# Optimization experiments

Hardware: AMD Instinct MI355X
Metric: run time of the kernel (lower is better)

Reference implementation:

```python
import jax, jax.numpy as jnp
import numpy as np

N = 50000      # num nodes
E = 800000     # num edges
F = 64         # in_channels
H = 4          # heads
C = 64         # out_channels
NEG_SLOPE = 0.2
SCALE = float(np.sqrt(F))  # scaled_product=True -> divide by sqrt(in_channels)


def setup_inputs() -> dict:
    key = jax.random.key(0)
    k1, k2, k3, k4, k5, k6 = jax.random.split(key, 6)
    x = jax.random.normal(k1, (N, F), dtype=jnp.float32)
    edge_index = jax.random.randint(k2, (2, E), 0, N, dtype=jnp.int32)
    edge_weight = jax.random.uniform(k3, (E, 1), dtype=jnp.float32)
    # learned parameters (glorot-ish scale)
    W_lin = jax.random.normal(k4, (F, H * C), dtype=jnp.float32) / np.sqrt(F)
    W_att = jax.random.normal(k5, (F, H * F), dtype=jnp.float32) / np.sqrt(F)
    bias = jnp.zeros((H * C,), dtype=jnp.float32)
    return {"x": x, "edge_index": edge_index, "edge_weight": edge_weight,
            "W_lin": W_lin, "W_att": W_att, "bias": bias}


def reference(x, edge_index, edge_weight, W_lin, W_att, bias):
    src = edge_index[0]  # j: source / message sender
    dst = edge_index[1]  # i: target / aggregation index

    # node transforms
    xs = (x @ W_lin).reshape(N, H, C)   # lin(x): values for messages
    u = (x @ W_att).reshape(N, H, F)    # lin_att(x): multiplicative attention keys

    # multiplicative attention score: x_j^T W_h x_i  -> [E, H]
    score = jnp.einsum('ehf,ef->eh', u[src], x[dst]) / SCALE
    score = jax.nn.leaky_relu(score, NEG_SLOPE)

    # masked scatter-softmax over incoming edges of each destination node
    smax = jax.ops.segment_max(jax.lax.stop_gradient(score), dst, num_segments=N)  # [N, H]
    e = jnp.exp(score - smax[dst]) * edge_weight                                   # mask = edge_weight
    denom = jax.ops.segment_sum(e, dst, num_segments=N) + 1e-16                    # [N, H]
    alpha = e / denom[dst]                                                         # [E, H]

    # message = alpha * x_src, aggregate (add) at destination
    out = jax.ops.segment_sum(alpha[:, :, None] * xs[src], dst, num_segments=N)    # [N, H, C]
    out = out.reshape(N, H * C) + bias                                             # concat heads + bias
    return out
```

## Files before the change

### kernel.cpp

```cpp
#include <hip/hip_runtime.h>
#include <hip/hip_bf16.h>
#include <math.h>

#define N_NODES 50000
#define N_EDGES 800000
#define GEMM_ROWS 32
#define AGG_NODES 32
#define PAD_EDGES (N_EDGES + N_NODES * 15)
#define QGEMM_BLOCKS ((N_NODES + GEMM_ROWS - 1) / GEMM_ROWS)
#define BASE_BLOCKS ((N_NODES + 255) / 256)
#define SCALE_FOLD 0.18033688011112042f
#define XT_STRIDE 36

typedef __attribute__((ext_vector_type(8))) short bf16x8_t;
typedef __attribute__((ext_vector_type(4))) float f32x4_t;

static __device__ __forceinline__ ushort bfrn(float v) {
  __hip_bfloat16 b = __float2bfloat16(v);
  return __builtin_bit_cast(ushort, b);
}
static __device__ __forceinline__ bf16x8_t as_bf16x8(uint4 u) {
  union { uint4 a; bf16x8_t b; } c; c.a = u; return c.b;
}
static __device__ __forceinline__ float bflo(uint u) {
  return __uint_as_float(u << 16);
}
static __device__ __forceinline__ float bfhi(uint u) {
  return __uint_as_float(u & 0xFFFF0000u);
}

__global__ __launch_bounds__(256) void hist_kernel(
    const int* __restrict__ dst, int* __restrict__ deg, int* __restrict__ epos,
    const float* __restrict__ Watt, float* __restrict__ Wt) {
  int e = blockIdx.x * 256 + threadIdx.x;
  if (e < 16384) {
    int c = e & 63;
    int r = (e >> 6) & 63;
    int h = e >> 12;
    Wt[e] = Watt[c * 256 + h * 64 + r] * SCALE_FOLD;
  }
  if (e < N_EDGES) epos[e] = atomicAdd(&deg[dst[e]], 1);
}

__global__ __launch_bounds__(256) void qgemm_base_kernel(
    const float* __restrict__ x, const float* __restrict__ Wt,
    uint2* __restrict__ q_t2, ushort* __restrict__ xhi,
    const int* __restrict__ deg, int* __restrict__ cursor,
    int2* __restrict__ offs2, int2* __restrict__ csr2) {
  const int tid = threadIdx.x;
  if (blockIdx.x >= QGEMM_BLOCKS) {
    const int i = (blockIdx.x - QGEMM_BLOCKS) * 256 + tid;
    const int lane = tid & 63;
    const int d = (i < N_NODES) ? deg[i] : 0;
    const int nt = (d + 15) >> 4;
    const int pd = nt << 4;
    int incl = pd;
#pragma unroll
    for (int m = 1; m < 64; m <<= 1) {
      int u = __shfl_up(incl, m);
      if (lane >= m) incl += u;
    }
    int wbase = 0;
    if (lane == 63) wbase = atomicAdd(cursor, incl);
    wbase = __shfl(wbase, 63);
    const int base = wbase + incl - pd;
    if (i < N_NODES) {
      offs2[i] = make_int2(base, nt);
      for (int j = d; j < pd; ++j) csr2[base + j] = make_int2(0, 0);
    }
    return;
  }
  __shared__ float xlds[GEMM_ROWS * 64];
  const int blk = blockIdx.x;
#pragma unroll
  for (int p = 0; p < 8; ++p) {
    int idx = p * 256 + tid;
    int gidx = blk * (GEMM_ROWS * 64) + idx;
    xlds[idx] = (gidx < N_NODES * 64) ? x[gidx] : 0.f;
  }
  __syncthreads();
  {
    int row = tid >> 3;
    int c0 = (tid & 7) * 8;
    int grow = blk * GEMM_ROWS + row;
    if (grow < N_NODES) {
      uint hu[4];
#pragma unroll
      for (int d2 = 0; d2 < 4; ++d2) {
        float v0 = xlds[row * 64 + c0 + 2 * d2];
        float v1 = xlds[row * 64 + c0 + 2 * d2 + 1];
        hu[d2] = (uint)bfrn(v0) | ((uint)bfrn(v1) << 16);
      }
      *(uint4*)(xhi + (size_t)grow * 64 + c0) =
          make_uint4(hu[0], hu[1], hu[2], hu[3]);
    }
  }
  const int c4 = tid & 63;
  const int h = c4 >> 4;
  const int f4 = c4 & 15;
  const int rg = (tid >> 6) * 8;
  const float4* Wv = (const float4*)Wt;
  float4 acc[8] = {};
  for (int g = 0; g < 64; ++g) {
    float4 w4 = Wv[(size_t)h * 1024 + g * 16 + f4];
#pragma unroll
    for (int r = 0; r < 8; ++r) {
      float a = xlds[(rg + r) * 64 + g];
      acc[r].x += a * w4.x; acc[r].y += a * w4.y;
      acc[r].z += a * w4.z; acc[r].w += a * w4.w;
    }
  }
#pragma unroll
  for (int r = 0; r < 8; ++r) {
    int row = blk * GEMM_ROWS + rg + r;
    if (row < N_NODES) {
      uint2 pk;
      pk.x = (uint)bfrn(acc[r].x) | ((uint)bfrn(acc[r].y) << 16);
      pk.y = (uint)bfrn(acc[r].z) | ((uint)bfrn(acc[r].w) << 16);
      q_t2[(size_t)row * 64 + c4] = pk;
    }
  }
}

__global__ __launch_bounds__(256) void scatter_kernel(
    const int* __restrict__ src, const int* __restrict__ dst,
    const float* __restrict__ ew, const int2* __restrict__ offs2,
    const int* __restrict__ epos, int2* __restrict__ csr2) {
  int e = blockIdx.x * 256 + threadIdx.x;
  if (e >= N_EDGES) return;
  int idx = offs2[dst[e]].x + epos[e];
  csr2[idx] = make_int2(src[e], __float_as_int(ew[e]));
}

__global__ __launch_bounds__(256) void aggregate_kernel(
    const uint4* __restrict__ qt4, const uint4* __restrict__ xhi4,
    const int2* __restrict__ offs2, const int2* __restrict__ csr2,
    ushort* __restrict__ agg) {
  __shared__ __attribute__((aligned(16))) uint xt[4][16][XT_STRIDE];
  __shared__ __attribute__((aligned(16))) float plds[4][16][4];
  const int wave = threadIdx.x >> 6;
  const int node = blockIdx.x * 4 + wave;
  const int lane = threadIdx.x & 63;
  const int l15 = lane & 15;
  const int lg = lane >> 4;
  const int hq = l15 & 3;

  const bf16x8_t Qa =
      as_bf16x8(qt4[(size_t)node * 32 + hq * 8 + lg]);
  const bf16x8_t Qb =
      as_bf16x8(qt4[(size_t)node * 32 + hq * 8 + 4 + lg]);
  const int2 o2 = offs2[node];
  const int s0 = o2.x;
  const int ntiles = o2.y;

  f32x4_t acc = {0.f, 0.f, 0.f, 0.f};
  float Lp = 0.f;

  for (int t = 0; t < ntiles; ++t) {
    const int k0 = s0 + t * 16;
    const int2 e2 = csr2[k0 + l15];
    const int j = e2.x;
    const float w = __int_as_float(e2.y);
    const uint4 ah0 = xhi4[(size_t)j * 8 + lg];
    const uint4 ah1 = xhi4[(size_t)j * 8 + 4 + lg];
    *(uint4*)&xt[wave][l15][4 * lg] = ah0;
    *(uint4*)&xt[wave][l15][16 + 4 * lg] = ah1;
    f32x4_t S = {0.f, 0.f, 0.f, 0.f};
    S = __builtin_amdgcn_mfma_f32_16x16x32_bf16(Qa, as_bf16x8(ah0), S, 0, 0, 0);
    S = __builtin_amdgcn_mfma_f32_16x16x32_bf16(Qb, as_bf16x8(ah1), S, 0, 0, 0);
    float p0 = exp2f(fmaxf(S[0], 0.2f * S[0])) * w;
    float p1 = exp2f(fmaxf(S[1], 0.2f * S[1])) * w;
    float p2 = exp2f(fmaxf(S[2], 0.2f * S[2])) * w;
    float p3 = exp2f(fmaxf(S[3], 0.2f * S[3])) * w;
    if (lg == 0) *(float4*)&plds[wave][l15][0] = make_float4(p0, p1, p2, p3);
#pragma unroll
    for (int e = 0; e < 16; ++e) {
      uint2 xw = *(const uint2*)&xt[wave][e][2 * l15];
      float pe = plds[wave][e][lg];
      acc[0] += pe * bflo(xw.x);
      acc[1] += pe * bfhi(xw.x);
      acc[2] += pe * bflo(xw.y);
      acc[3] += pe * bfhi(xw.y);
      Lp += pe;
    }
  }

  const float inv = 1.f / (Lp + 1e-16f);
  uint w0 = (uint)bfrn(acc[0] * inv) | ((uint)bfrn(acc[1] * inv) << 16);
  uint w1 = (uint)bfrn(acc[2] * inv) | ((uint)bfrn(acc[3] * inv) << 16);
  *(uint2*)(agg + (size_t)node * 256 + lg * 64 + l15 * 4) = make_uint2(w0, w1);
}

__global__ __launch_bounds__(256) void out_gemm_kernel(
    const ushort* __restrict__ agg, const float* __restrict__ Wlin,
    const float* __restrict__ bias, float* __restrict__ out) {
  __shared__ float4 atile[AGG_NODES][4][17];
  const int tid = threadIdx.x;
  const int node0 = blockIdx.x * AGG_NODES;
  const uint2* av = (const uint2*)agg;
#pragma unroll
  for (int p = 0; p < 8; ++p) {
    int idx = p * 256 + tid;
    int row = idx >> 6;
    int cc = idx & 63;
    if (node0 + row < N_NODES) {
      uint2 u = av[(size_t)(node0 + row) * 64 + cc];
      float4 f;
      f.x = bflo(u.x); f.y = bfhi(u.x);
      f.z = bflo(u.y); f.w = bfhi(u.y);
      atile[row][cc >> 4][cc & 15] = f;
    }
  }
  __syncthreads();
  const int c4 = tid & 63;
  const int ns = tid >> 6;
  const int hh = c4 >> 4;
  const float4* Wv = (const float4*)Wlin;
  float4 acc[8] = {};
  for (int g4 = 0; g4 < 16; ++g4) {
    float4 w0 = Wv[(size_t)(g4 * 4 + 0) * 64 + c4];
    float4 w1 = Wv[(size_t)(g4 * 4 + 1) * 64 + c4];
    float4 w2 = Wv[(size_t)(g4 * 4 + 2) * 64 + c4];
    float4 w3 = Wv[(size_t)(g4 * 4 + 3) * 64 + c4];
#pragma unroll
    for (int n = 0; n < 8; ++n) {
      float4 a = atile[ns * 8 + n][hh][g4];
      acc[n].x += a.x * w0.x + a.y * w1.x + a.z * w2.x + a.w * w3.x;
      acc[n].y += a.x * w0.y + a.y * w1.y + a.z * w2.y + a.w * w3.y;
      acc[n].z += a.x * w0.z + a.y * w1.z + a.z * w2.z + a.w * w3.z;
      acc[n].w += a.x * w0.w + a.y * w1.w + a.z * w2.w + a.w * w3.w;
    }
  }
  float4 bv = ((const float4*)bias)[c4];
#pragma unroll
  for (int n = 0; n < 8; ++n) {
    int node = node0 + ns * 8 + n;
    if (node < N_NODES) {
      float4 o;
      o.x = acc[n].x + bv.x; o.y = acc[n].y + bv.y;
      o.z = acc[n].z + bv.z; o.w = acc[n].w + bv.w;
      ((float4*)out)[(size_t)node * 64 + c4] = o;
    }
  }
}

extern "C" void kernel_launch(void* const* d_in, const int* in_sizes, int n_in,
                              void* d_out, int out_size, void* d_ws,
                              size_t ws_size, hipStream_t stream) {
  (void)in_sizes; (void)n_in; (void)out_size; (void)ws_size;
  const float* x    = (const float*)d_in[0];
  const int*   ei   = (const int*)d_in[1];
  const float* ew   = (const float*)d_in[2];
  const float* Wlin = (const float*)d_in[3];
  const float* Watt = (const float*)d_in[4];
  const float* bias = (const float*)d_in[5];
  float* out = (float*)d_out;

  const int* srcv = ei;
  const int* dstv = ei + N_EDGES;

  char* ws = (char*)d_ws;
  size_t off = 0;
  auto alloc = [&](size_t bytes) {
    void* p = ws + off;
    off += (bytes + 255) & ~(size_t)255;
    return p;
  };
  ushort* q_t   = (ushort*)alloc((size_t)N_NODES * 256 * 2);
  ushort* agg   = (ushort*)alloc((size_t)N_NODES * 256 * 2);
  ushort* xhi   = (ushort*)alloc((size_t)N_NODES * 64 * 2);
  int2*   offs2 = (int2*)alloc((size_t)N_NODES * 8);
  int2*   csr2  = (int2*)alloc((size_t)PAD_EDGES * 8);
  char* aggc = (char*)agg;
  int*   deg    = (int*)aggc;
  int*   cursor = (int*)(aggc + N_NODES * 4);
  int*   epos   = (int*)(aggc + 256 * 1024);
  float* Wt     = (float*)(aggc + 4 * 1024 * 1024);

  hipMemsetAsync(deg, 0, (size_t)(N_NODES + 64) * 4, stream);

  hist_kernel<<<(N_EDGES + 255) / 256, 256, 0, stream>>>(dstv, deg, epos,
                                                         Watt, Wt);
  qgemm_base_kernel<<<QGEMM_BLOCKS + BASE_BLOCKS, 256, 0, stream>>>(
      x, Wt, (uint2*)q_t, xhi, deg, cursor, offs2, csr2);
  scatter_kernel<<<(N_EDGES + 255) / 256, 256, 0, stream>>>(
      srcv, dstv, ew, offs2, epos, csr2);
  aggregate_kernel<<<N_NODES / 4, 256, 0, stream>>>(
      (const uint4*)q_t, (const uint4*)xhi, offs2, csr2, agg);
  out_gemm_kernel<<<(N_NODES + AGG_NODES - 1) / AGG_NODES, 256, 0, stream>>>(
      agg, Wlin, bias, out);
}
```

Baseline: 170.9 us.

## Fuse all pipeline stages into one cooperative persistent kernel with grid syncs

Replaces the memset plus five kernel launches with a single cooperative mega-kernel. It uses grid-wide syncs between the histogram, scan, q-GEMM/scatter, aggregate and output-GEMM phases, and loops persistently over virtual blocks. The aim is to remove launch overhead and the gaps between kernels. In exchange, grid size is capped at 1024 blocks, so occupancy is limited, and each phase carries grid.sync cost. The old multi-kernel path stays as a fallback if the cooperative launch fails.

```diff
diff --git a/kernel.cpp b/kernel.cpp
--- a/kernel.cpp
+++ b/kernel.cpp
@@ -1,6 +1,9 @@
 #include <hip/hip_runtime.h>
+#include <hip/hip_cooperative_groups.h>
 #include <hip/hip_bf16.h>
 #include <math.h>
+
+namespace cg = cooperative_groups;
 
 #define N_NODES 50000
 #define N_EDGES 800000
@@ -8,7 +11,12 @@
 #define AGG_NODES 32
 #define PAD_EDGES (N_EDGES + N_NODES * 15)
 #define QGEMM_BLOCKS ((N_NODES + GEMM_ROWS - 1) / GEMM_ROWS)
+#define SCAT_CHUNKS ((N_EDGES + 255) / 256)
 #define BASE_BLOCKS ((N_NODES + 255) / 256)
+#define AGG_VB (N_NODES / 4)
+#define OUT_VB (N_NODES / 16)
+#define GRID_WANT 1024
+#define NUM_CU 256
 #define SCALE_FOLD 0.18033688011112042f
 #define XT_STRIDE 36
 
@@ -27,6 +35,234 @@
 }
 static __device__ __forceinline__ float bfhi(uint u) {
   return __uint_as_float(u & 0xFFFF0000u);
+}
+
+__global__ __launch_bounds__(256) void mega_kernel(
+    const float* __restrict__ x, const int* __restrict__ srcv,
+    const int* __restrict__ dstv, const float* __restrict__ ew,
+    const float* __restrict__ Wlin, const float* __restrict__ bias,
+    const float* __restrict__ Watt, float* __restrict__ out,
+    ushort* __restrict__ q_t, ushort* __restrict__ xhi,
+    ushort* __restrict__ agg, int2* __restrict__ offs2,
+    int2* __restrict__ csr2, int* __restrict__ deg,
+    int* __restrict__ cursor, int* __restrict__ epos,
+    float* __restrict__ Wt) {
+  __shared__ __attribute__((aligned(16))) char pool[17408];
+  cg::grid_group grid = cg::this_grid();
+  const int tid = threadIdx.x;
+  const int bid = blockIdx.x;
+  const int nblk = gridDim.x;
+  const int gtid = bid * 256 + tid;
+  const int gthreads = nblk * 256;
+  const int lane = tid & 63;
+  const int wave = tid >> 6;
+
+  for (int i = gtid; i < N_NODES; i += gthreads) deg[i] = 0;
+  if (gtid == 0) cursor[0] = 0;
+  __threadfence();
+  grid.sync();
+
+  if (gtid < 16384) {
+    int c = gtid & 63, r = (gtid >> 6) & 63, h = gtid >> 12;
+    Wt[gtid] = Watt[c * 256 + h * 64 + r] * SCALE_FOLD;
+  }
+  for (int e = gtid; e < N_EDGES; e += gthreads)
+    epos[e] = atomicAdd(&deg[dstv[e]], 1);
+  __threadfence();
+  grid.sync();
+
+  if (bid < BASE_BLOCKS) {
+    const int i = gtid;
+    const int d = (i < N_NODES) ? deg[i] : 0;
+    const int nt = (d + 15) >> 4;
+    const int pd = nt << 4;
+    int incl = pd;
+#pragma unroll
+    for (int m = 1; m < 64; m <<= 1) {
+      int u = __shfl_up(incl, m);
+      if (lane >= m) incl += u;
+    }
+    int wbase = 0;
+    if (lane == 63) wbase = atomicAdd(cursor, incl);
+    wbase = __shfl(wbase, 63);
+    const int base = wbase + incl - pd;
+    if (i < N_NODES) {
+      offs2[i] = make_int2(base, nt);
+      for (int j = d; j < pd; ++j) csr2[base + j] = make_int2(0, 0);
+    }
+  }
+  __threadfence();
+  grid.sync();
+
+  for (int vb = bid; vb < QGEMM_BLOCKS + SCAT_CHUNKS; vb += nblk) {
+    if (vb < QGEMM_BLOCKS) {
+      float* xlds = (float*)pool;
+      __syncthreads();
+#pragma unroll
+      for (int p = 0; p < 8; ++p) {
+        int idx = p * 256 + tid;
+        int gidx = vb * (GEMM_ROWS * 64) + idx;
+        xlds[idx] = (gidx < N_NODES * 64) ? x[gidx] : 0.f;
+      }
+      __syncthreads();
+      {
+        int row = tid >> 3;
+        int c0 = (tid & 7) * 8;
+        int grow = vb * GEMM_ROWS + row;
+        if (grow < N_NODES) {
+          uint hu[4];
+#pragma unroll
+          for (int d2 = 0; d2 < 4; ++d2) {
+            float v0 = xlds[row * 64 + c0 + 2 * d2];
+            float v1 = xlds[row * 64 + c0 + 2 * d2 + 1];
+            hu[d2] = (uint)bfrn(v0) | ((uint)bfrn(v1) << 16);
+          }
+          *(uint4*)(xhi + (size_t)grow * 64 + c0) =
+              make_uint4(hu[0], hu[1], hu[2], hu[3]);
+        }
+      }
+      const int c4 = tid & 63;
+      const int h = c4 >> 4;
+      const int f4 = c4 & 15;
+      const int rg = (tid >> 6) * 8;
+      const float4* Wv = (const float4*)Wt;
+      float4 acc[8] = {};
+      for (int g = 0; g < 64; ++g) {
+        float4 w4 = Wv[(size_t)h * 1024 + g * 16 + f4];
+#pragma unroll
+        for (int r = 0; r < 8; ++r) {
+          float a = xlds[(rg + r) * 64 + g];
+          acc[r].x += a * w4.x; acc[r].y += a * w4.y;
+          acc[r].z += a * w4.z; acc[r].w += a * w4.w;
+        }
+      }
+      uint2* q_t2 = (uint2*)q_t;
+#pragma unroll
+      for (int r = 0; r < 8; ++r) {
+        int row = vb * GEMM_ROWS + rg + r;
+        if (row < N_NODES) {
+          uint2 pk;
+          pk.x = (uint)bfrn(acc[r].x) | ((uint)bfrn(acc[r].y) << 16);
+          pk.y = (uint)bfrn(acc[r].z) | ((uint)bfrn(acc[r].w) << 16);
+          q_t2[(size_t)row * 64 + c4] = pk;
+        }
+      }
+    } else {
+      int e = (vb - QGEMM_BLOCKS) * 256 + tid;
+      if (e < N_EDGES) {
+        int idx = offs2[dstv[e]].x + epos[e];
+        csr2[idx] = make_int2(srcv[e], __float_as_int(ew[e]));
+      }
+    }
+  }
+  __threadfence();
+  grid.sync();
+
+  {
+    auto xt = (uint(*)[16][XT_STRIDE])pool;
+    auto plds = (float(*)[16][4])(pool + 9216);
+    const uint4* qt4 = (const uint4*)q_t;
+    const uint4* xhi4 = (const uint4*)xhi;
+    const int l15 = lane & 15;
+    const int lg = lane >> 4;
+    const int hq = l15 & 3;
+    for (int vb = bid; vb < AGG_VB; vb += nblk) {
+      const int node = vb * 4 + wave;
+      const bf16x8_t Qa = as_bf16x8(qt4[(size_t)node * 32 + hq * 8 + lg]);
+      const bf16x8_t Qb = as_bf16x8(qt4[(size_t)node * 32 + hq * 8 + 4 + lg]);
+      const int2 o2 = offs2[node];
+      const int s0 = o2.x;
+      const int ntiles = o2.y;
+      f32x4_t acc = {0.f, 0.f, 0.f, 0.f};
+      float Lp = 0.f;
+      for (int t = 0; t < ntiles; ++t) {
+        const int k0 = s0 + t * 16;
+        const int2 e2 = csr2[k0 + l15];
+        const int j = e2.x;
+        const float w = __int_as_float(e2.y);
+        const uint4 ah0 = xhi4[(size_t)j * 8 + lg];
+        const uint4 ah1 = xhi4[(size_t)j * 8 + 4 + lg];
+        *(uint4*)&xt[wave][l15][4 * lg] = ah0;
+        *(uint4*)&xt[wave][l15][16 + 4 * lg] = ah1;
+        f32x4_t S = {0.f, 0.f, 0.f, 0.f};
+        S = __builtin_amdgcn_mfma_f32_16x16x32_bf16(Qa, as_bf16x8(ah0), S, 0,
+                                                    0, 0);
+        S = __builtin_amdgcn_mfma_f32_16x16x32_bf16(Qb, as_bf16x8(ah1), S, 0,
+                                                    0, 0);
+        float p0 = exp2f(fmaxf(S[0], 0.2f * S[0])) * w;
+        float p1 = exp2f(fmaxf(S[1], 0.2f * S[1])) * w;
+        float p2 = exp2f(fmaxf(S[2], 0.2f * S[2])) * w;
+        float p3 = exp2f(fmaxf(S[3], 0.2f * S[3])) * w;
+        if (lg == 0)
+          *(float4*)&plds[wave][l15][0] = make_float4(p0, p1, p2, p3);
+#pragma unroll
+        for (int e = 0; e < 16; ++e) {
+          uint2 xw = *(const uint2*)&xt[wave][e][2 * l15];
+          float pe = plds[wave][e][lg];
+          acc[0] += pe * bflo(xw.x);
+          acc[1] += pe * bfhi(xw.x);
+          acc[2] += pe * bflo(xw.y);
+          acc[3] += pe * bfhi(xw.y);
+          Lp += pe;
+        }
+      }
+      const float inv = 1.f / (Lp + 1e-16f);
+      uint w0 = (uint)bfrn(acc[0] * inv) | ((uint)bfrn(acc[1] * inv) << 16);
+      uint w1 = (uint)bfrn(acc[2] * inv) | ((uint)bfrn(acc[3] * inv) << 16);
+      *(uint2*)(agg + (size_t)node * 256 + lg * 64 + l15 * 4) =
+          make_uint2(w0, w1);
+    }
+  }
+  __threadfence();
+  grid.sync();
+
+  {
+    auto atile = (float4(*)[4][17])pool;
+    const uint2* av = (const uint2*)agg;
+    const int c4 = tid & 63;
+    const int grp = tid >> 6;
+    const int hh = c4 >> 4;
+    const float4* Wv = (const float4*)Wlin;
+    const float4 bv = ((const float4*)bias)[c4];
+    for (int vb = bid; vb < OUT_VB; vb += nblk) {
+      const int node0 = vb * 16;
+      __syncthreads();
+#pragma unroll
+      for (int p = 0; p < 4; ++p) {
+        int idx = p * 256 + tid;
+        int row = idx >> 6;
+        int cc = idx & 63;
+        uint2 u = av[(size_t)(node0 + row) * 64 + cc];
+        float4 f;
+        f.x = bflo(u.x); f.y = bfhi(u.x);
+        f.z = bflo(u.y); f.w = bfhi(u.y);
+        atile[row][cc >> 4][cc & 15] = f;
+      }
+      __syncthreads();
+      float4 acc[4] = {};
+      for (int g4 = 0; g4 < 16; ++g4) {
+        float4 w0 = Wv[(size_t)(g4 * 4 + 0) * 64 + c4];
+        float4 w1 = Wv[(size_t)(g4 * 4 + 1) * 64 + c4];
+        float4 w2 = Wv[(size_t)(g4 * 4 + 2) * 64 + c4];
+        float4 w3 = Wv[(size_t)(g4 * 4 + 3) * 64 + c4];
+#pragma unroll
+        for (int n = 0; n < 4; ++n) {
+          float4 a = atile[grp * 4 + n][hh][g4];
+          acc[n].x += a.x * w0.x + a.y * w1.x + a.z * w2.x + a.w * w3.x;
+          acc[n].y += a.x * w0.y + a.y * w1.y + a.z * w2.y + a.w * w3.y;
+          acc[n].z += a.x * w0.z + a.y * w1.z + a.z * w2.z + a.w * w3.z;
+          acc[n].w += a.x * w0.w + a.y * w1.w + a.z * w2.w + a.w * w3.w;
+        }
+      }
+#pragma unroll
+      for (int n = 0; n < 4; ++n) {
+        float4 o;
+        o.x = acc[n].x + bv.x; o.y = acc[n].y + bv.y;
+        o.z = acc[n].z + bv.z; o.w = acc[n].w + bv.w;
+        ((float4*)out)[(size_t)(node0 + grp * 4 + n) * 64 + c4] = o;
+      }
+    }
+  }
 }
 
 __global__ __launch_bounds__(256) void hist_kernel(
@@ -144,18 +380,13 @@
   const int l15 = lane & 15;
   const int lg = lane >> 4;
   const int hq = l15 & 3;
-
-  const bf16x8_t Qa =
-      as_bf16x8(qt4[(size_t)node * 32 + hq * 8 + lg]);
-  const bf16x8_t Qb =
-      as_bf16x8(qt4[(size_t)node * 32 + hq * 8 + 4 + lg]);
+  const bf16x8_t Qa = as_bf16x8(qt4[(size_t)node * 32 + hq * 8 + lg]);
+  const bf16x8_t Qb = as_bf16x8(qt4[(size_t)node * 32 + hq * 8 + 4 + lg]);
   const int2 o2 = offs2[node];
   const int s0 = o2.x;
   const int ntiles = o2.y;
-
   f32x4_t acc = {0.f, 0.f, 0.f, 0.f};
   float Lp = 0.f;
-
   for (int t = 0; t < ntiles; ++t) {
     const int k0 = s0 + t * 16;
     const int2 e2 = csr2[k0 + l15];
@@ -184,7 +415,6 @@
       Lp += pe;
     }
   }
-
   const float inv = 1.f / (Lp + 1e-16f);
   uint w0 = (uint)bfrn(acc[0] * inv) | ((uint)bfrn(acc[1] * inv) << 16);
   uint w1 = (uint)bfrn(acc[2] * inv) | ((uint)bfrn(acc[3] * inv) << 16);
@@ -277,8 +507,25 @@
   int*   epos   = (int*)(aggc + 256 * 1024);
   float* Wt     = (float*)(aggc + 4 * 1024 * 1024);
 
+  int maxBlocksPerCU = 0;
+  hipError_t qerr = hipOccupancyMaxActiveBlocksPerMultiprocessor(
+      &maxBlocksPerCU, (const void*)mega_kernel, 256, 0);
+  bool coop_done = false;
+  if (qerr == hipSuccess && maxBlocksPerCU >= 1) {
+    int gridsz = maxBlocksPerCU * NUM_CU;
+    if (gridsz > GRID_WANT) gridsz = GRID_WANT;
+    if (gridsz >= 256) {
+      void* args[] = {&x,    &srcv, &dstv, &ew,    &Wlin, &bias,   &Watt,
+                      &out,  &q_t,  &xhi,  &agg,   &offs2, &csr2,  &deg,
+                      &cursor, &epos, &Wt};
+      hipError_t lerr = hipLaunchCooperativeKernel(
+          (const void*)mega_kernel, dim3(gridsz), dim3(256), args, 0, stream);
+      coop_done = (lerr == hipSuccess);
+    }
+  }
+  if (coop_done) return;
+
   hipMemsetAsync(deg, 0, (size_t)(N_NODES + 64) * 4, stream);
-
   hist_kernel<<<(N_EDGES + 255) / 256, 256, 0, stream>>>(dstv, deg, epos,
                                                          Watt, Wt);
   qgemm_base_kernel<<<QGEMM_BLOCKS + BASE_BLOCKS, 256, 0, stream>>>(
```

New measurement: 170.8 us. Within noise of the previous version (-0.1%).

## Replace scalar attention-weighted aggregation loop with bf16 MFMA accumulation

Applied to the files above, without the earlier changes.

The per-tile aggregation of 16 edge messages, previously done as a scalar FMA loop over LDS-staged features, is now expressed as a 16x16x32 bf16 MFMA: the attention weights are rounded to bf16 and stored transposed in LDS as the A operand, and gathered x rows are repacked into per-column B operands. The softmax denominator is also computed with an MFMA against a ones vector. The aim is to cut VALU work and LDS reads in the hot loop. In exchange the attention probabilities lose precision, LDS traffic shifts to 16-bit scattered reads, and half of each MFMA's K dimension is zero-padded.

```diff
diff --git a/kernel.cpp b/kernel.cpp
--- a/kernel.cpp
+++ b/kernel.cpp
@@ -10,7 +10,7 @@
 #define QGEMM_BLOCKS ((N_NODES + GEMM_ROWS - 1) / GEMM_ROWS)
 #define BASE_BLOCKS ((N_NODES + 255) / 256)
 #define SCALE_FOLD 0.18033688011112042f
-#define XT_STRIDE 36
+#define XT_STRIDE 34
 
 typedef __attribute__((ext_vector_type(8))) short bf16x8_t;
 typedef __attribute__((ext_vector_type(4))) float f32x4_t;
@@ -136,8 +136,8 @@
     const uint4* __restrict__ qt4, const uint4* __restrict__ xhi4,
     const int2* __restrict__ offs2, const int2* __restrict__ csr2,
     ushort* __restrict__ agg) {
-  __shared__ __attribute__((aligned(16))) uint xt[4][16][XT_STRIDE];
-  __shared__ __attribute__((aligned(16))) float plds[4][16][4];
+  __shared__ __attribute__((aligned(16))) ushort xt16[4][16][XT_STRIDE * 2];
+  __shared__ __attribute__((aligned(16))) ushort pt[4][4][16];
   const int wave = threadIdx.x >> 6;
   const int node = blockIdx.x * 4 + wave;
   const int lane = threadIdx.x & 63;
@@ -145,16 +145,21 @@
   const int lg = lane >> 4;
   const int hq = l15 & 3;
 
-  const bf16x8_t Qa =
-      as_bf16x8(qt4[(size_t)node * 32 + hq * 8 + lg]);
-  const bf16x8_t Qb =
-      as_bf16x8(qt4[(size_t)node * 32 + hq * 8 + 4 + lg]);
+  const bf16x8_t Qa = as_bf16x8(qt4[(size_t)node * 32 + hq * 8 + lg]);
+  const bf16x8_t Qb = as_bf16x8(qt4[(size_t)node * 32 + hq * 8 + 4 + lg]);
   const int2 o2 = offs2[node];
   const int s0 = o2.x;
   const int ntiles = o2.y;
 
-  f32x4_t acc = {0.f, 0.f, 0.f, 0.f};
-  float Lp = 0.f;
+  const bf16x8_t ONES =
+      as_bf16x8(make_uint4(0x3F803F80u, 0x3F803F80u, 0x3F803F80u, 0x3F803F80u));
+  f32x4_t acc0 = {0.f, 0.f, 0.f, 0.f};
+  f32x4_t acc1 = {0.f, 0.f, 0.f, 0.f};
+  f32x4_t acc2 = {0.f, 0.f, 0.f, 0.f};
+  f32x4_t acc3 = {0.f, 0.f, 0.f, 0.f};
+  f32x4_t accL = {0.f, 0.f, 0.f, 0.f};
+
+  const int eb = (lg & 1) * 8;
 
   for (int t = 0; t < ntiles; ++t) {
     const int k0 = s0 + t * 16;
@@ -163,8 +168,13 @@
     const float w = __int_as_float(e2.y);
     const uint4 ah0 = xhi4[(size_t)j * 8 + lg];
     const uint4 ah1 = xhi4[(size_t)j * 8 + 4 + lg];
-    *(uint4*)&xt[wave][l15][4 * lg] = ah0;
-    *(uint4*)&xt[wave][l15][16 + 4 * lg] = ah1;
+    {
+      ushort* xr = &xt16[wave][l15][0];
+      *(uint2*)(xr + 8 * lg) = make_uint2(ah0.x, ah0.y);
+      *(uint2*)(xr + 8 * lg + 4) = make_uint2(ah0.z, ah0.w);
+      *(uint2*)(xr + 32 + 8 * lg) = make_uint2(ah1.x, ah1.y);
+      *(uint2*)(xr + 32 + 8 * lg + 4) = make_uint2(ah1.z, ah1.w);
+    }
     f32x4_t S = {0.f, 0.f, 0.f, 0.f};
     S = __builtin_amdgcn_mfma_f32_16x16x32_bf16(Qa, as_bf16x8(ah0), S, 0, 0, 0);
     S = __builtin_amdgcn_mfma_f32_16x16x32_bf16(Qb, as_bf16x8(ah1), S, 0, 0, 0);
@@ -172,23 +182,56 @@
     float p1 = exp2f(fmaxf(S[1], 0.2f * S[1])) * w;
     float p2 = exp2f(fmaxf(S[2], 0.2f * S[2])) * w;
     float p3 = exp2f(fmaxf(S[3], 0.2f * S[3])) * w;
-    if (lg == 0) *(float4*)&plds[wave][l15][0] = make_float4(p0, p1, p2, p3);
-#pragma unroll
-    for (int e = 0; e < 16; ++e) {
-      uint2 xw = *(const uint2*)&xt[wave][e][2 * l15];
-      float pe = plds[wave][e][lg];
-      acc[0] += pe * bflo(xw.x);
-      acc[1] += pe * bfhi(xw.x);
-      acc[2] += pe * bflo(xw.y);
-      acc[3] += pe * bfhi(xw.y);
-      Lp += pe;
-    }
-  }
-
-  const float inv = 1.f / (Lp + 1e-16f);
-  uint w0 = (uint)bfrn(acc[0] * inv) | ((uint)bfrn(acc[1] * inv) << 16);
-  uint w1 = (uint)bfrn(acc[2] * inv) | ((uint)bfrn(acc[3] * inv) << 16);
-  *(uint2*)(agg + (size_t)node * 256 + lg * 64 + l15 * 4) = make_uint2(w0, w1);
+    if (lg == 0) {
+      pt[wave][0][l15] = bfrn(p0);
+      pt[wave][1][l15] = bfrn(p1);
+      pt[wave][2][l15] = bfrn(p2);
+      pt[wave][3][l15] = bfrn(p3);
+    }
+    uint4 pau = make_uint4(0u, 0u, 0u, 0u);
+    if (lg < 2) pau = *(const uint4*)&pt[wave][hq][8 * lg];
+    const bf16x8_t pa = as_bf16x8(pau);
+#pragma unroll
+    for (int b = 0; b < 4; ++b) {
+      const int fc = 16 * b + l15;
+      uint bw0 = (uint)xt16[wave][eb + 0][fc] |
+                 ((uint)xt16[wave][eb + 1][fc] << 16);
+      uint bw1 = (uint)xt16[wave][eb + 2][fc] |
+                 ((uint)xt16[wave][eb + 3][fc] << 16);
+      uint bw2 = (uint)xt16[wave][eb + 4][fc] |
+                 ((uint)xt16[wave][eb + 5][fc] << 16);
+      uint bw3 = (uint)xt16[wave][eb + 6][fc] |
+                 ((uint)xt16[wave][eb + 7][fc] << 16);
+      const bf16x8_t bx = as_bf16x8(make_uint4(bw0, bw1, bw2, bw3));
+      if (b == 0)
+        acc0 = __builtin_amdgcn_mfma_f32_16x16x32_bf16(pa, bx, acc0, 0, 0, 0);
+      else if (b == 1)
+        acc1 = __builtin_amdgcn_mfma_f32_16x16x32_bf16(pa, bx, acc1, 0, 0, 0);
+      else if (b == 2)
+        acc2 = __builtin_amdgcn_mfma_f32_16x16x32_bf16(pa, bx, acc2, 0, 0, 0);
+      else
+        acc3 = __builtin_amdgcn_mfma_f32_16x16x32_bf16(pa, bx, acc3, 0, 0, 0);
+    }
+    accL = __builtin_amdgcn_mfma_f32_16x16x32_bf16(pa, ONES, accL, 0, 0, 0);
+  }
+
+  const float lpv = (lg == 0) ? accL[0]
+                  : (lg == 1) ? accL[1]
+                  : (lg == 2) ? accL[2] : accL[3];
+  const float inv = 1.f / (lpv + 1e-16f);
+  const float v0 = ((lg == 0) ? acc0[0] : (lg == 1) ? acc0[1]
+                   : (lg == 2) ? acc0[2] : acc0[3]) * inv;
+  const float v1 = ((lg == 0) ? acc1[0] : (lg == 1) ? acc1[1]
+                   : (lg == 2) ? acc1[2] : acc1[3]) * inv;
+  const float v2 = ((lg == 0) ? acc2[0] : (lg == 1) ? acc2[1]
+                   : (lg == 2) ? acc2[2] : acc2[3]) * inv;
+  const float v3 = ((lg == 0) ? acc3[0] : (lg == 1) ? acc3[1]
+                   : (lg == 2) ? acc3[2] : acc3[3]) * inv;
+  ushort* ap = agg + (size_t)node * 256 + lg * 64 + l15;
+  ap[0] = bfrn(v0);
+  ap[16] = bfrn(v1);
+  ap[32] = bfrn(v2);
+  ap[48] = bfrn(v3);
 }
 
 __global__ __launch_bounds__(256) void out_gemm_kernel(
```

Result: no change. 171.1 us (+0.1%).
